# Optimization experiments

Measured on AMD Instinct MI355X. Metric: run time of the kernel, lower is better.

## Reference

```python
import jax, jax.numpy as jnp
import numpy as np


def _nn_mean_sqdist(source, target):
    # source: [N,3], target: [M,3]
    s_norm = jnp.sum(source ** 2, axis=1, keepdims=True)          # [N,1]
    t_norm = jnp.sum(target ** 2, axis=1, keepdims=True)          # [M,1]
    dist = s_norm + t_norm.T - 2.0 * (source @ target.T)          # [N,M] squared dists
    return jnp.min(dist, axis=1).mean()


def setup_inputs() -> dict:
    key = jax.random.key(0)
    k1, k2 = jax.random.split(key)
    pred_positions = jax.random.normal(k1, (16384, 3), dtype=jnp.float32)
    target_positions = jax.random.normal(k2, (16384, 3), dtype=jnp.float32)
    return {"pred_positions": pred_positions, "target_positions": target_positions}


def reference(pred_positions, target_positions):
    d_pt = _nn_mean_sqdist(pred_positions, target_positions)
    d_tp = _nn_mean_sqdist(target_positions, pred_positions)  # use_bidirectional=True
    return (d_pt + d_tp) / 2.0
```

## Files before the change

### kernel.cpp

```cpp
#include <hip/hip_runtime.h>

#define TPB 256
#define R 8
#define CHUNKS 64

__global__ __launch_bounds__(TPB) void prep_kernel(
        const float* __restrict__ a, const float* __restrict__ b,
        float4* __restrict__ pa, float4* __restrict__ pb,
        unsigned* __restrict__ pmins, float* __restrict__ acc,
        unsigned* __restrict__ cnt, int n) {
    int idx = blockIdx.x * blockDim.x + threadIdx.x;
    if (idx < n) {
        float x = a[3 * idx], y = a[3 * idx + 1], z = a[3 * idx + 2];
        pa[idx] = make_float4(x, y, z, x * x + y * y + z * z);
    } else if (idx < 2 * n) {
        int i = idx - n;
        float x = b[3 * i], y = b[3 * i + 1], z = b[3 * i + 2];
        pb[i] = make_float4(x, y, z, x * x + y * y + z * z);
    }
    if (idx < 2 * n) pmins[idx] = 0xFFFFFFFFu;
    if (idx == 0) { acc[0] = 0.0f; cnt[0] = 0u; }
}

__global__ __launch_bounds__(TPB, 4) void minpass_kernel(
        const float4* __restrict__ pa, const float4* __restrict__ pb,
        unsigned* __restrict__ pmins, int n) {
    const int SB = n / (TPB * R);
    const int CH = n / CHUNKS;
    int b = blockIdx.x;
    int dir = b / (SB * CHUNKS);
    int rem = b % (SB * CHUNKS);
    int chunk = rem / SB;
    int sblk = rem % SB;
    const float4* __restrict__ src = dir ? pb : pa;
    const float4* __restrict__ tgt = dir ? pa : pb;

    __shared__ float4 tile[256];
    int base = chunk * CH;
    for (int i = threadIdx.x; i < CH; i += TPB)
        tile[i] = tgt[base + i];

    float ax[R], ay[R], az[R], sw[R], m[R];
    int s0 = sblk * TPB * R + threadIdx.x;
#pragma unroll
    for (int r = 0; r < R; ++r) {
        float4 s = src[s0 + r * TPB];
        ax[r] = -2.0f * s.x; ay[r] = -2.0f * s.y; az[r] = -2.0f * s.z;
        sw[r] = s.w; m[r] = __builtin_inff();
    }
    __syncthreads();

#pragma unroll 4
    for (int j = 0; j < CH; j += 2) {
        float4 p0 = tile[j];
        float4 p1 = tile[j + 1];
#pragma unroll
        for (int r = 0; r < R; ++r) {
            float d0 = fmaf(ax[r], p0.x, fmaf(ay[r], p0.y, fmaf(az[r], p0.z, p0.w)));
            float d1 = fmaf(ax[r], p1.x, fmaf(ay[r], p1.y, fmaf(az[r], p1.z, p1.w)));
            m[r] = fminf(m[r], fminf(d0, d1));
        }
    }

#pragma unroll
    for (int r = 0; r < R; ++r)
        atomicMin(&pmins[dir * n + s0 + r * TPB], __float_as_uint(m[r] + sw[r]));
}

__global__ __launch_bounds__(TPB) void finalize_kernel(
        const uint4* __restrict__ pmins, float* __restrict__ acc,
        unsigned* __restrict__ cnt, float* __restrict__ out, int n, int nblocks) {
    int i = blockIdx.x * TPB + threadIdx.x;
    uint4 v = pmins[i];
    float sum = __uint_as_float(v.x) + __uint_as_float(v.y)
              + __uint_as_float(v.z) + __uint_as_float(v.w);
    for (int off = 32; off > 0; off >>= 1)
        sum += __shfl_down(sum, off, 64);
    __shared__ float wsum[TPB / 64];
    int lane = threadIdx.x & 63, wid = threadIdx.x >> 6;
    if (lane == 0) wsum[wid] = sum;
    __syncthreads();
    if (threadIdx.x == 0) {
        float t = 0.0f;
        for (int w = 0; w < TPB / 64; ++w) t += wsum[w];
        atomicAdd(acc, t);
        __threadfence();
        unsigned old = atomicAdd(cnt, 1u);
        if (old == (unsigned)(nblocks - 1)) {
            float a0 = atomicAdd(acc, 0.0f);
            out[0] = a0 / (float)(2 * n);
        }
    }
}

extern "C" void kernel_launch(void* const* d_in, const int* in_sizes, int n_in,
                              void* d_out, int out_size, void* d_ws, size_t ws_size,
                              hipStream_t stream) {
    const float* a = (const float*)d_in[0];
    const float* b = (const float*)d_in[1];
    int n = in_sizes[0] / 3;
    float* out = (float*)d_out;
    char* ws = (char*)d_ws;
    float* acc = (float*)ws;
    unsigned* cnt = (unsigned*)(ws + 8);
    float4* pa = (float4*)(ws + 256);
    float4* pb = pa + n;
    unsigned* pmins = (unsigned*)(ws + 256 + 2 * (size_t)n * sizeof(float4));

    prep_kernel<<<(2 * n + TPB - 1) / TPB, TPB, 0, stream>>>(
        a, b, pa, pb, pmins, acc, cnt, n);
    int SB = n / (TPB * R);
    minpass_kernel<<<2 * SB * CHUNKS, TPB, 0, stream>>>(pa, pb, pmins, n);
    int fblocks = (2 * n / 4) / TPB;
    finalize_kernel<<<fblocks, TPB, 0, stream>>>(
        (const uint4*)pmins, acc, cnt, out, n, fblocks);
}
```

Baseline: 98.82 us.

## Compute pairwise distances with bf16 split-precision MFMA instead of scalar FMAs

Reformulates the squared-distance computation as a matrix product on the 32x32x16 bf16 MFMA units. Each coordinate is split into hi/lo bf16 parts and the norm into three bf16 parts, which recovers near-fp32 accuracy. Target tiles are double-buffered in swizzled shared memory, and row minima are reduced across lanes with shuffles before the atomicMin. The goal is to move the dominant O(N^2) FMA work onto matrix cores, at the cost of extra packing work and some risk of precision loss in the min-distance results.

```diff
diff --git a/kernel.cpp b/kernel.cpp
--- a/kernel.cpp
+++ b/kernel.cpp
@@ -1,70 +1,153 @@
 #include <hip/hip_runtime.h>
 
 #define TPB 256
-#define R 8
-#define CHUNKS 64
+
+typedef __attribute__((ext_vector_type(8))) short bf16x8;
+typedef __attribute__((ext_vector_type(16))) float f32x16;
+
+__device__ inline unsigned short f2bf(float f) {
+    unsigned u = __float_as_uint(f);
+    return (unsigned short)((u + 0x7FFFu + ((u >> 16) & 1u)) >> 16);
+}
+__device__ inline float bf2f(unsigned short h) {
+    return __uint_as_float((unsigned)h << 16);
+}
+__device__ inline uint4 pack8(unsigned short s0, unsigned short s1,
+                              unsigned short s2, unsigned short s3,
+                              unsigned short s4, unsigned short s5,
+                              unsigned short s6, unsigned short s7) {
+    uint4 v;
+    v.x = (unsigned)s0 | ((unsigned)s1 << 16);
+    v.y = (unsigned)s2 | ((unsigned)s3 << 16);
+    v.z = (unsigned)s4 | ((unsigned)s5 << 16);
+    v.w = (unsigned)s6 | ((unsigned)s7 << 16);
+    return v;
+}
+__device__ inline bf16x8 as_frag(uint4 v) {
+    union { uint4 u; bf16x8 f; } c; c.u = v; return c.f;
+}
 
 __global__ __launch_bounds__(TPB) void prep_kernel(
         const float* __restrict__ a, const float* __restrict__ b,
-        float4* __restrict__ pa, float4* __restrict__ pb,
-        unsigned* __restrict__ pmins, float* __restrict__ acc,
-        unsigned* __restrict__ cnt, int n) {
-    int idx = blockIdx.x * blockDim.x + threadIdx.x;
-    if (idx < n) {
-        float x = a[3 * idx], y = a[3 * idx + 1], z = a[3 * idx + 2];
-        pa[idx] = make_float4(x, y, z, x * x + y * y + z * z);
-    } else if (idx < 2 * n) {
-        int i = idx - n;
-        float x = b[3 * i], y = b[3 * i + 1], z = b[3 * i + 2];
-        pb[i] = make_float4(x, y, z, x * x + y * y + z * z);
-    }
-    if (idx < 2 * n) pmins[idx] = 0xFFFFFFFFu;
+        uint4* __restrict__ pAa, uint4* __restrict__ pBa,
+        uint4* __restrict__ pAb, uint4* __restrict__ pBb,
+        float* __restrict__ norms, unsigned* __restrict__ pmins,
+        float* __restrict__ acc, unsigned* __restrict__ cnt, int n) {
+    int idx = blockIdx.x * TPB + threadIdx.x;
+    if (idx < 2 * n) {
+        int isB = idx >= n;
+        int i = isB ? idx - n : idx;
+        const float* s = isB ? b : a;
+        float x = s[3 * i], y = s[3 * i + 1], z = s[3 * i + 2];
+        float w = x * x + y * y + z * z;
+        norms[idx] = w;
+        float ax = -2.0f * x, ay = -2.0f * y, az = -2.0f * z;
+        unsigned short ahx = f2bf(ax), ahy = f2bf(ay), ahz = f2bf(az);
+        unsigned short alx = f2bf(ax - bf2f(ahx));
+        unsigned short aly = f2bf(ay - bf2f(ahy));
+        unsigned short alz = f2bf(az - bf2f(ahz));
+        unsigned short thx = f2bf(x), thy = f2bf(y), thz = f2bf(z);
+        unsigned short tlx = f2bf(x - bf2f(thx));
+        unsigned short tly = f2bf(y - bf2f(thy));
+        unsigned short tlz = f2bf(z - bf2f(thz));
+        unsigned short wh = f2bf(w);  float r1 = w - bf2f(wh);
+        unsigned short wm = f2bf(r1); float r2 = r1 - bf2f(wm);
+        unsigned short wl = f2bf(r2);
+        const unsigned short ONE = 0x3F80;
+        uint4* Ad = (isB ? pAb : pAa) + (size_t)i * 2;
+        uint4* Bd = (isB ? pBb : pBa) + (size_t)i * 2;
+        Ad[0] = pack8(ahx, ahy, ahz, alx, aly, alz, ahx, ahy);
+        Ad[1] = pack8(ahz, ONE, ONE, ONE, alx, aly, alz, 0);
+        Bd[0] = pack8(thx, thy, thz, thx, thy, thz, tlx, tly);
+        Bd[1] = pack8(tlz, wh, wm, wl, tlx, tly, tlz, 0);
+        pmins[idx] = 0xFFFFFFFFu;
+    }
     if (idx == 0) { acc[0] = 0.0f; cnt[0] = 0u; }
 }
 
-__global__ __launch_bounds__(TPB, 4) void minpass_kernel(
-        const float4* __restrict__ pa, const float4* __restrict__ pb,
-        unsigned* __restrict__ pmins, int n) {
-    const int SB = n / (TPB * R);
-    const int CH = n / CHUNKS;
-    int b = blockIdx.x;
-    int dir = b / (SB * CHUNKS);
-    int rem = b % (SB * CHUNKS);
-    int chunk = rem / SB;
-    int sblk = rem % SB;
-    const float4* __restrict__ src = dir ? pb : pa;
-    const float4* __restrict__ tgt = dir ? pa : pb;
-
-    __shared__ float4 tile[256];
-    int base = chunk * CH;
-    for (int i = threadIdx.x; i < CH; i += TPB)
-        tile[i] = tgt[base + i];
-
-    float ax[R], ay[R], az[R], sw[R], m[R];
-    int s0 = sblk * TPB * R + threadIdx.x;
-#pragma unroll
-    for (int r = 0; r < R; ++r) {
-        float4 s = src[s0 + r * TPB];
-        ax[r] = -2.0f * s.x; ay[r] = -2.0f * s.y; az[r] = -2.0f * s.z;
-        sw[r] = s.w; m[r] = __builtin_inff();
-    }
+__global__ __launch_bounds__(TPB, 3) void minpass_kernel(
+        const uint4* __restrict__ pAa, const uint4* __restrict__ pBa,
+        const uint4* __restrict__ pAb, const uint4* __restrict__ pBb,
+        const float* __restrict__ norms, unsigned* __restrict__ pmins, int n) {
+    const int NSG = n / 256;
+    const int TS = 4;
+    const int TGT = n / TS;
+    const int NCH = TGT / 128;
+
+    int bid = blockIdx.x;
+    int dir = bid / (NSG * TS);
+    int rem = bid % (NSG * TS);
+    int sg = rem / TS;
+    int ts = rem % TS;
+
+    const uint4* __restrict__ Ap = dir ? pAb : pAa;
+    const uint4* __restrict__ Bp = dir ? pBa : pBb;
+
+    __shared__ uint4 buf[2][256];
+
+    const int tid = threadIdx.x;
+    const int wid = tid >> 6, lane = tid & 63;
+    const int lr = lane & 31, lh = lane >> 5;
+    const int bidx = ((lr << 1) | lh) ^ ((lr >> 2) & 7);
+    const int wslot = tid ^ ((tid >> 3) & 7);
+
+    int row0 = sg * 256 + wid * 32 + lr;
+    bf16x8 a0 = as_frag(Ap[(size_t)row0 * 2 + lh]);
+    bf16x8 a1 = as_frag(Ap[(size_t)(row0 + 128) * 2 + lh]);
+
+    float rm0[16], rm1[16];
+#pragma unroll
+    for (int i = 0; i < 16; ++i) { rm0[i] = __builtin_inff(); rm1[i] = __builtin_inff(); }
+    f32x16 z = {};
+
+    const int tbase = ts * TGT;
+    uint4 pf = Bp[(size_t)tbase * 2 + tid];
+    buf[0][wslot] = pf;
     __syncthreads();
 
-#pragma unroll 4
-    for (int j = 0; j < CH; j += 2) {
-        float4 p0 = tile[j];
-        float4 p1 = tile[j + 1];
-#pragma unroll
-        for (int r = 0; r < R; ++r) {
-            float d0 = fmaf(ax[r], p0.x, fmaf(ay[r], p0.y, fmaf(az[r], p0.z, p0.w)));
-            float d1 = fmaf(ax[r], p1.x, fmaf(ay[r], p1.y, fmaf(az[r], p1.z, p1.w)));
-            m[r] = fminf(m[r], fminf(d0, d1));
-        }
-    }
-
-#pragma unroll
-    for (int r = 0; r < R; ++r)
-        atomicMin(&pmins[dir * n + s0 + r * TPB], __float_as_uint(m[r] + sw[r]));
+    for (int ch = 0; ch < NCH; ++ch) {
+        const int cur = ch & 1;
+        uint4 nf;
+        if (ch + 1 < NCH) nf = Bp[(size_t)(tbase + (ch + 1) * 128) * 2 + tid];
+        const uint4* lb = buf[cur];
+#pragma unroll
+        for (int t = 0; t < 4; t += 2) {
+            bf16x8 b0 = as_frag(lb[t * 64 + bidx]);
+            bf16x8 b1 = as_frag(lb[t * 64 + 64 + bidx]);
+            f32x16 d00 = __builtin_amdgcn_mfma_f32_32x32x16_bf16(a0, b0, z, 0, 0, 0);
+            f32x16 d10 = __builtin_amdgcn_mfma_f32_32x32x16_bf16(a1, b0, z, 0, 0, 0);
+            f32x16 d01 = __builtin_amdgcn_mfma_f32_32x32x16_bf16(a0, b1, z, 0, 0, 0);
+            f32x16 d11 = __builtin_amdgcn_mfma_f32_32x32x16_bf16(a1, b1, z, 0, 0, 0);
+#pragma unroll
+            for (int i = 0; i < 16; ++i) {
+                rm0[i] = fminf(rm0[i], fminf(d00[i], d01[i]));
+                rm1[i] = fminf(rm1[i], fminf(d10[i], d11[i]));
+            }
+        }
+        if (ch + 1 < NCH) buf[cur ^ 1][wslot] = nf;
+        __syncthreads();
+    }
+
+#pragma unroll
+    for (int k = 1; k < 32; k <<= 1) {
+#pragma unroll
+        for (int i = 0; i < 16; ++i) {
+            rm0[i] = fminf(rm0[i], __shfl_xor(rm0[i], k, 64));
+            rm1[i] = fminf(rm1[i], __shfl_xor(rm1[i], k, 64));
+        }
+    }
+    if (lr == 0) {
+        unsigned* pm = pmins + (size_t)dir * n;
+        const float* nb = norms + (dir ? n : 0);
+        int rb = sg * 256 + wid * 32 + lh * 4;
+#pragma unroll
+        for (int i = 0; i < 16; ++i) {
+            int r = (i & 3) + ((i >> 2) << 3);
+            int r0 = rb + r, r1 = rb + 128 + r;
+            atomicMin(&pm[r0], __float_as_uint(rm0[i] + nb[r0]));
+            atomicMin(&pm[r1], __float_as_uint(rm1[i] + nb[r1]));
+        }
+    }
 }
 
 __global__ __launch_bounds__(TPB) void finalize_kernel(
@@ -103,14 +186,20 @@
     char* ws = (char*)d_ws;
     float* acc = (float*)ws;
     unsigned* cnt = (unsigned*)(ws + 8);
-    float4* pa = (float4*)(ws + 256);
-    float4* pb = pa + n;
-    unsigned* pmins = (unsigned*)(ws + 256 + 2 * (size_t)n * sizeof(float4));
+    float* norms = (float*)(ws + 256);
+    char* packs = ws + 256 + (size_t)2 * n * 4;
+    size_t psz = (size_t)n * 32;
+    uint4* pAa = (uint4*)(packs);
+    uint4* pBa = (uint4*)(packs + psz);
+    uint4* pAb = (uint4*)(packs + 2 * psz);
+    uint4* pBb = (uint4*)(packs + 3 * psz);
+    unsigned* pmins = (unsigned*)(packs + 4 * psz);
 
     prep_kernel<<<(2 * n + TPB - 1) / TPB, TPB, 0, stream>>>(
-        a, b, pa, pb, pmins, acc, cnt, n);
-    int SB = n / (TPB * R);
-    minpass_kernel<<<2 * SB * CHUNKS, TPB, 0, stream>>>(pa, pb, pmins, n);
+        a, b, pAa, pBa, pAb, pBb, norms, pmins, acc, cnt, n);
+    int mblocks = 2 * (n / 256) * 4;
+    minpass_kernel<<<mblocks, TPB, 0, stream>>>(
+        pAa, pBa, pAb, pBb, norms, pmins, n);
     int fblocks = (2 * n / 4) / TPB;
     finalize_kernel<<<fblocks, TPB, 0, stream>>>(
         (const uint4*)pmins, acc, cnt, out, n, fblocks);
```

New measurement: 123.2 us. +24.7%, slower.
